# Optimization experiments

Measured on AMD Instinct MI355X. Metric: run time of the kernel, lower is better.

The kernel has to match this reference:

```python
import jax, jax.numpy as jnp
import numpy as np

B, L, S = 1, 2048, 2048
D_MODEL, H = 1024, 16
DK = D_MODEL // H  # d_keys = d_values = 64


def sparsemax(z):
    # sparsemax along last axis: proj of z onto the simplex
    K = z.shape[-1]
    z_sorted = jnp.flip(jnp.sort(z, axis=-1), axis=-1)
    cs = jnp.cumsum(z_sorted, axis=-1)
    r = jnp.arange(1, K + 1, dtype=z.dtype)
    support = 1.0 + r * z_sorted > cs
    k = jnp.sum(support, axis=-1, keepdims=True)
    tau = (jnp.take_along_axis(cs, k.astype(jnp.int32) - 1, axis=-1) - 1.0) / k.astype(z.dtype)
    return jnp.maximum(z - tau, 0.0)


def setup_inputs() -> dict:
    key = jax.random.key(0)
    ks = jax.random.split(key, 12)
    sc = 1.0 / np.sqrt(D_MODEL)
    return {
        "queries": jax.random.normal(ks[0], (B, L, D_MODEL), jnp.float32),
        "keys": jax.random.normal(ks[1], (B, S, D_MODEL), jnp.float32),
        "values": jax.random.normal(ks[2], (B, S, D_MODEL), jnp.float32),
        "Wq": jax.random.normal(ks[3], (D_MODEL, H * DK), jnp.float32) * sc,
        "bq": jnp.zeros((H * DK,), jnp.float32),
        "Wk": jax.random.normal(ks[4], (D_MODEL, H * DK), jnp.float32) * sc,
        "bk": jnp.zeros((H * DK,), jnp.float32),
        "Wv": jax.random.normal(ks[5], (H * DK, H * DK), jnp.float32) * sc,
        "bv": jnp.zeros((H * DK,), jnp.float32),
        "Wo": jax.random.normal(ks[6], (H * DK, D_MODEL), jnp.float32) * sc,
        "bo": jnp.zeros((D_MODEL,), jnp.float32),
    }


def reference(queries, keys, values, Wq, bq, Wk, bk, Wv, bv, Wo, bo):
    # projections (note: input `values` is unused, matching the torch source)
    q = (queries @ Wq + bq).reshape(B, L, H, DK)
    k_flat = keys @ Wk + bk                      # [B,S,H*DK]
    k = k_flat.reshape(B, S, H, DK)
    v = (k_flat @ Wv + bv).reshape(B, S, H, DK)  # value_projection(key_projection(keys))
    scale = 1.0 / np.sqrt(DK)
    scores = jnp.einsum('blhe,bshe->bhls', q, k) * scale  # [B,H,L,S]
    A = sparsemax(scores)
    out = jnp.einsum('bhls,bshd->blhd', A, v)             # [B,L,H,DK]
    # mix=True: transpose(2,1) -> [B,H,L,D] then view(B,L,-1)
    out = jnp.swapaxes(out, 1, 2).reshape(B, L, H * DK)
    return out @ Wo + bo
```

## Files before the change

### kernel.cpp

```cpp
#include <hip/hip_runtime.h>
#include <hip/hip_bf16.h>


typedef __attribute__((ext_vector_type(8))) short short8;
typedef __attribute__((ext_vector_type(4))) float floatx4;

#define SRC_BF16 0
#define SRC_F32  1
#define SRC_RT   2
#define NSEG 3
#define OVF 64
#define CAPT (64 * NSEG + OVF)

typedef __attribute__((address_space(1))) const void GAS;
typedef __attribute__((address_space(3))) void LAS;
#define GLOAD16(g, l) __builtin_amdgcn_global_load_lds((GAS*)(g), (LAS*)(l), 16, 0, 0)

__device__ __forceinline__ short f2bf(float f) {
    __hip_bfloat16 h = __float2bfloat16(f);
    return *reinterpret_cast<const short*>(&h);
}
__device__ __forceinline__ unsigned short f2bfu(float f) {
    __hip_bfloat16 h = __float2bfloat16(f);
    return *reinterpret_cast<const unsigned short*>(&h);
}
__device__ __forceinline__ float bf2f(unsigned short u) {
    return __uint_as_float(((unsigned)u) << 16);
}
__device__ __forceinline__ unsigned fmap(float f) {
    unsigned u = __float_as_uint(f);
    return (u & 0x80000000u) ? ~u : (u | 0x80000000u);
}
__device__ __forceinline__ float funmap(unsigned u) {
    return (u & 0x80000000u) ? __uint_as_float(u ^ 0x80000000u) : __uint_as_float(~u);
}

__global__ void detect_k(const short* __restrict__ q, int n, int* __restrict__ flag)
{
    const int tid = threadIdx.x;
    int bad = 0;
    for (int i = tid; i < n; i += 64) {
        float f = bf2f((unsigned short)q[i]);
        if (!(fabsf(f) < 1e10f)) bad = 1;
    }
    unsigned long long m = __ballot(bad != 0);
    if (tid == 0) *flag = (m != 0ULL) ? 1 : 0;
}

__global__ __launch_bounds__(256)
void convert2_k(const void* __restrict__ s0, const void* __restrict__ s1,
                short* __restrict__ d0, short* __restrict__ d1,
                const int* __restrict__ dflag)
{
    const void* s = blockIdx.z ? s1 : s0;
    short* d = blockIdx.z ? d1 : d0;
    const size_t i = ((size_t)blockIdx.x * 256 + threadIdx.x) * 8;
    short8 o;
    if (*dflag) {
        const float4 f0 = ((const float4*)((const float*)s + i))[0];
        const float4 f1 = ((const float4*)((const float*)s + i))[1];
        o[0] = f2bf(f0.x); o[1] = f2bf(f0.y); o[2] = f2bf(f0.z); o[3] = f2bf(f0.w);
        o[4] = f2bf(f1.x); o[5] = f2bf(f1.y); o[6] = f2bf(f1.z); o[7] = f2bf(f1.w);
    } else {
        o = *(const short8*)((const short*)s + i);
    }
    *(short8*)(d + i) = o;
}

struct TP4 {
    const void* s[4];
    short* d[4];
};
__global__ __launch_bounds__(256)
void transpose4_k(TP4 p, int R, int C, const int* __restrict__ dflag)
{
    __shared__ short T[64][72];
    const int tid = threadIdx.x;
    const int bC = blockIdx.x, bR = blockIdx.y;
    const void* src = p.s[blockIdx.z];
    short* dst = p.d[blockIdx.z];
    const bool f32 = (*dflag != 0);

    const int colg = (tid & 7) * 8;
    #pragma unroll
    for (int h = 0; h < 2; ++h) {
        const int row = (tid >> 3) + 32 * h;
        const size_t idx = (size_t)(bR * 64 + row) * (size_t)C + (size_t)(bC * 64 + colg);
        short e[8];
        if (f32) {
            const float4 f0 = ((const float4*)((const float*)src + idx))[0];
            const float4 f1 = ((const float4*)((const float*)src + idx))[1];
            e[0] = f2bf(f0.x); e[1] = f2bf(f0.y); e[2] = f2bf(f0.z); e[3] = f2bf(f0.w);
            e[4] = f2bf(f1.x); e[5] = f2bf(f1.y); e[6] = f2bf(f1.z); e[7] = f2bf(f1.w);
        } else {
            short8 s = *(const short8*)((const short*)src + idx);
            #pragma unroll
            for (int j = 0; j < 8; ++j) e[j] = s[j];
        }
        #pragma unroll
        for (int j = 0; j < 8; ++j) T[colg + j][row] = e[j];
    }
    __syncthreads();
    #pragma unroll
    for (int h = 0; h < 2; ++h) {
        const int orow = (tid >> 3) + 32 * h;
        const int ocolg = (tid & 7) * 8;
        const size_t idx = (size_t)(bC * 64 + orow) * (size_t)R + (size_t)(bR * 64 + ocolg);
        *(short8*)(dst + idx) = *(const short8*)&T[orow][ocolg];
    }
}

struct GJ { const short* A; const short* B; const void* bias; void* C; float os; };

template<int OSRC>
__global__ __launch_bounds__(256)
void gemm64_bt_k(GJ j0, GJ j1, const int* __restrict__ dflag)
{
    __shared__ __align__(16) short As[2][64][64];
    __shared__ __align__(16) short Bs[2][64][64];

    const GJ j = blockIdx.z ? j1 : j0;
    const int rtf = *dflag;

    const int tid  = threadIdx.x;
    const int bN   = blockIdx.x, bM = blockIdx.y;
    const int lane = tid & 63, wave = tid >> 6;
    const int wm   = (wave >> 1) * 32;
    const int wn   = (wave & 1) * 32;
    const int quad = lane >> 4, r16 = lane & 15;

    floatx4 acc[2][2];
    #pragma unroll
    for (int i = 0; i < 2; ++i)
        #pragma unroll
        for (int jj = 0; jj < 2; ++jj)
            acc[i][jj] = (floatx4){0.f, 0.f, 0.f, 0.f};

    const int srow = wave * 8 + (lane >> 3);
    const int scg  = (lane & 7) ^ ((lane >> 3) & 7);
    const short* gA = j.A + (size_t)(bM * 64 + srow) * 1024 + scg * 8;
    const short* gB = j.B + (size_t)(bN * 64 + srow) * 1024 + scg * 8;

#define STAGE(buf, k0)                                                          \
    {                                                                           \
        _Pragma("unroll")                                                       \
        for (int jj = 0; jj < 2; ++jj) {                                        \
            GLOAD16(gA + (size_t)jj * 32 * 1024 + (k0),                         \
                    &As[buf][wave * 8 + jj * 32][0]);                           \
            GLOAD16(gB + (size_t)jj * 32 * 1024 + (k0),                         \
                    &Bs[buf][wave * 8 + jj * 32][0]);                           \
        }                                                                       \
    }

    STAGE(0, 0);
    __syncthreads();

    const int sr = r16 & 7;
    int buf = 0;
    for (int t = 0; t < 16; ++t) {
        if (t < 15) STAGE(buf ^ 1, (t + 1) * 64);
        #pragma unroll
        for (int kk = 0; kk < 2; ++kk) {
            const int pc = ((kk * 4 + quad) ^ sr) * 8;
            const short8 a0 = *(const short8*)&As[buf][wm + r16][pc];
            const short8 a1 = *(const short8*)&As[buf][wm + 16 + r16][pc];
            const short8 b0 = *(const short8*)&Bs[buf][wn + r16][pc];
            const short8 b1 = *(const short8*)&Bs[buf][wn + 16 + r16][pc];
            acc[0][0] = __builtin_amdgcn_mfma_f32_16x16x32_bf16(a0, b0, acc[0][0], 0, 0, 0);
            acc[0][1] = __builtin_amdgcn_mfma_f32_16x16x32_bf16(a0, b1, acc[0][1], 0, 0, 0);
            acc[1][0] = __builtin_amdgcn_mfma_f32_16x16x32_bf16(a1, b0, acc[1][0], 0, 0, 0);
            acc[1][1] = __builtin_amdgcn_mfma_f32_16x16x32_bf16(a1, b1, acc[1][1], 0, 0, 0);
        }
        __syncthreads();
        buf ^= 1;
    }
#undef STAGE

    const bool of32 = (OSRC == SRC_F32) || (OSRC == SRC_RT && rtf);
    #pragma unroll
    for (int jj = 0; jj < 2; ++jj) {
        const int gc = bN * 64 + wn + jj * 16 + r16;
        const float bb = rtf ? ((const float*)j.bias)[gc]
                             : bf2f(((const unsigned short*)j.bias)[gc]);
        #pragma unroll
        for (int i = 0; i < 2; ++i) {
            #pragma unroll
            for (int rg = 0; rg < 4; ++rg) {
                const int gr = bM * 64 + wm + i * 16 + quad * 4 + rg;
                const float v = (acc[i][jj][rg] + bb) * j.os;
                if (of32)
                    ((float*)j.C)[(size_t)gr * 1024 + gc] = v;
                else
                    ((__hip_bfloat16*)j.C)[(size_t)gr * 1024 + gc] = __float2bfloat16(v);
            }
        }
    }
}

__global__ __launch_bounds__(256, 8)
void attn_fused_k(const short* __restrict__ Qb, const short* __restrict__ Kb,
                  const short* __restrict__ Vb, short* __restrict__ Ob)
{
    __shared__ unsigned cpk[16][CAPT];
    __shared__ unsigned rmax[16];
    __shared__ int cnt[16];

    const int tid  = threadIdx.x;
    const int lane = tid & 63, wave = tid >> 6;
    const int quad = lane >> 4, r16 = lane & 15;

    const int bid  = blockIdx.x;
    const int slot = bid >> 3;
    const int h    = (slot & 1) * 8 + (bid & 7);
    const int row0 = (slot >> 1) * 16;

    if (tid < 16) { rmax[tid] = fmap(-3.0e38f); cnt[tid] = 0; }
    __syncthreads();

    const short* qp = Qb + (size_t)(row0 + r16) * 1024 + h * 64 + quad * 8;
    const short8 qa0 = *(const short8*)qp;
    const short8 qa1 = *(const short8*)(qp + 32);

    const int myrow = quad * 4;
    const int wid   = wave * 16 + r16;
    const short* kp0 = Kb + (size_t)(wave * 16 + r16) * 1024 + h * 64 + quad * 8;

    float rm1[4], rm2[4];
    int mycnt[4];
    #pragma unroll
    for (int rg = 0; rg < 4; ++rg) { rm1[rg] = -3.0e38f; rm2[rg] = -3.0e38f; mycnt[rg] = 0; }

    for (int s0 = 0; s0 < 2048; s0 += 256) {
        floatx4 acc[4];
        #pragma unroll
        for (int t = 0; t < 4; ++t) {
            const short* kp = kp0 + (size_t)(s0 + t * 64) * 1024;
            const short8 b0 = *(const short8*)kp;
            const short8 b1 = *(const short8*)(kp + 32);
            floatx4 a = (floatx4){0.f, 0.f, 0.f, 0.f};
            a = __builtin_amdgcn_mfma_f32_16x16x32_bf16(qa0, b0, a, 0, 0, 0);
            a = __builtin_amdgcn_mfma_f32_16x16x32_bf16(qa1, b1, a, 0, 0, 0);
            acc[t] = a;
        }

        #pragma unroll
        for (int rg = 0; rg < 4; ++rg) {
            float m1ab = fmaxf(acc[0][rg], acc[1][rg]);
            float m2ab = fminf(acc[0][rg], acc[1][rg]);
            float m1cd = fmaxf(acc[2][rg], acc[3][rg]);
            float m2cd = fminf(acc[2][rg], acc[3][rg]);
            float m1 = fmaxf(m1ab, m1cd);
            float m2 = fmaxf(fminf(m1ab, m1cd), (m1ab >= m1cd) ? m2ab : m2cd);
            #pragma unroll
            for (int off = 1; off < 16; off <<= 1) {
                const float o1 = __shfl_xor(m1, off, 64);
                const float o2 = __shfl_xor(m2, off, 64);
                const float n2 = fmaxf(fminf(m1, o1), (m1 >= o1) ? m2 : o2);
                m1 = fmaxf(m1, o1);
                m2 = n2;
            }
            const float n1 = fmaxf(rm1[rg], m1);
            rm2[rg] = fmaxf(fminf(rm1[rg], m1), (rm1[rg] >= m1) ? rm2[rg] : m2);
            rm1[rg] = n1;
            if (r16 == 0) atomicMax(&rmax[myrow + rg], fmap(m1));
        }

        #pragma unroll
        for (int rg = 0; rg < 4; ++rg) {
            const int row = myrow + rg;
            const float g1 = fmaxf(funmap(rmax[row]), rm1[rg]);
            const float thr = fmaxf(g1 - 1.0f, 0.5f * (g1 + rm2[rg]) - 0.5f);
            #pragma unroll
            for (int t = 0; t < 4; ++t) {
                const float val = acc[t][rg];
                if (val >= thr) {
                    const unsigned pk = ((unsigned)f2bfu(val) << 16)
                                      | (unsigned)(s0 + wave * 16 + t * 64 + r16);
                    const int c = mycnt[rg];
                    if (c < NSEG) {
                        cpk[row][wid * NSEG + c] = pk;
                    } else {
                        const int p = atomicAdd(&cnt[row], 1);
                        if (p < OVF) cpk[row][64 * NSEG + p] = pk;
                    }
                    mycnt[rg] = c + 1;
                }
            }
        }
    }

    #pragma unroll
    for (int rg = 0; rg < 4; ++rg) {
        const int row = myrow + rg;
        for (int k = mycnt[rg]; k < NSEG; ++k)
            cpk[row][wid * NSEG + k] = 0xFF800000u;
    }
    __syncthreads();

    const int r = wave * 4 + quad;
    const int novf = min(cnt[r], OVF);

    unsigned ca[16];
    #pragma unroll
    for (int k = 0; k < 12; ++k) ca[k] = cpk[r][k * 16 + r16];
    #pragma unroll
    for (int k = 12; k < 16; ++k) {
        const int oi = k * 16 + r16 - 64 * NSEG;
        ca[k] = (oi < novf) ? cpk[r][k * 16 + r16] : 0xFF800000u;
    }

    float tau = funmap(rmax[r]) - 1.0f;
    float prevc = -1.0f;
    for (int it = 0; it < 18; ++it) {
        float s = 0.f, c = 0.f;
        #pragma unroll
        for (int k = 0; k < 16; ++k) {
            const float v = __uint_as_float(ca[k] & 0xFFFF0000u);
            if (v > tau) { s += v; c += 1.f; }
        }
        #pragma unroll
        for (int off = 1; off < 16; off <<= 1) {
            s += __shfl_xor(s, off, 64);
            c += __shfl_xor(c, off, 64);
        }
        if (c == prevc || c == 0.f) break;
        prevc = c;
        tau = (s - 1.0f) / c;
    }

    const unsigned qpre = (1u << r16) - 1u;
    int base = 0;
    #pragma unroll
    for (int k = 0; k < 16; ++k) {
        const float v = __uint_as_float(ca[k] & 0xFFFF0000u);
        const float p = v - tau;
        const bool keep = (p > 0.f);
        const unsigned long long mm = __ballot(keep);
        const unsigned qm = (unsigned)((mm >> (quad * 16)) & 0xFFFFull);
        if (keep)
            cpk[r][base + __popc(qm & qpre)] =
                ((unsigned)f2bfu(p) << 16) | (ca[k] & 0xFFFFu);
        base += __popc(qm);
    }
    const int msup = base;

    const unsigned short* vb = (const unsigned short*)Vb + (size_t)h * 64 + r16 * 4;
    float o0 = 0.f, o1 = 0.f, o2 = 0.f, o3 = 0.f;
    int jj = 0;
    for (; jj + 2 <= msup; jj += 2) {
        const unsigned ua = cpk[r][jj], ub = cpk[r][jj + 1];
        const float pa = __uint_as_float(ua & 0xFFFF0000u);
        const float pb = __uint_as_float(ub & 0xFFFF0000u);
        const uint2 da = *(const uint2*)(vb + (size_t)(ua & 0xFFFFu) * 1024);
        const uint2 db = *(const uint2*)(vb + (size_t)(ub & 0xFFFFu) * 1024);
        o0 += pa * __uint_as_float(da.x << 16);
        o1 += pa * __uint_as_float(da.x & 0xFFFF0000u);
        o2 += pa * __uint_as_float(da.y << 16);
        o3 += pa * __uint_as_float(da.y & 0xFFFF0000u);
        o0 += pb * __uint_as_float(db.x << 16);
        o1 += pb * __uint_as_float(db.x & 0xFFFF0000u);
        o2 += pb * __uint_as_float(db.y << 16);
        o3 += pb * __uint_as_float(db.y & 0xFFFF0000u);
    }
    if (jj < msup) {
        const unsigned ua = cpk[r][jj];
        const float pa = __uint_as_float(ua & 0xFFFF0000u);
        const uint2 da = *(const uint2*)(vb + (size_t)(ua & 0xFFFFu) * 1024);
        o0 += pa * __uint_as_float(da.x << 16);
        o1 += pa * __uint_as_float(da.x & 0xFFFF0000u);
        o2 += pa * __uint_as_float(da.y << 16);
        o3 += pa * __uint_as_float(da.y & 0xFFFF0000u);
    }

    short* op = Ob + ((size_t)h * 2048 + row0 + r) * 64 + r16 * 4;
    op[0] = f2bf(o0); op[1] = f2bf(o1); op[2] = f2bf(o2); op[3] = f2bf(o3);
}

extern "C" void kernel_launch(void* const* d_in, const int* in_sizes, int n_in,
                              void* d_out, int out_size, void* d_ws, size_t ws_size,
                              hipStream_t stream)
{
    (void)in_sizes; (void)n_in; (void)out_size; (void)ws_size;

    const void* queries = d_in[0];
    const void* keys    = d_in[1];
    const void* Wq = d_in[3];
    const void* bq = d_in[4];
    const void* Wk = d_in[5];
    const void* bk = d_in[6];
    const void* Wv = d_in[7];
    const void* bv = d_in[8];
    const void* Wo = d_in[9];
    const void* bo = d_in[10];

    const int L = 2048, DM = 1024;
    const size_t LD = (size_t)L * DM;

    int*   flag = (int*)d_ws;
    short* Qc  = (short*)((char*)d_ws + 256);
    short* Kc  = Qc + LD;
    short* WqT = Kc + LD;
    short* WkT = WqT + (size_t)DM * DM;
    short* WvT = WkT + (size_t)DM * DM;
    short* WoT = WvT + (size_t)DM * DM;
    short* Qb  = WoT + (size_t)DM * DM;
    short* Kb  = Qb + LD;
    short* Vb  = Kb + LD;
    short* Ob  = Vb + LD;

    dim3 blk(256);

    detect_k<<<dim3(1), dim3(64), 0, stream>>>((const short*)queries, 4096, flag);

    convert2_k<<<dim3((unsigned)(LD / 2048), 1, 2), blk, 0, stream>>>(
        queries, keys, Qc, Kc, flag);

    {
        TP4 p;
        p.s[0] = Wq; p.s[1] = Wk; p.s[2] = Wv; p.s[3] = Wo;
        p.d[0] = WqT; p.d[1] = WkT; p.d[2] = WvT; p.d[3] = WoT;
        transpose4_k<<<dim3(DM / 64, DM / 64, 4), blk, 0, stream>>>(p, DM, DM, flag);
    }

    {
        GJ jq{(const short*)Qc, WqT, bq, Qb, 0.125f};
        GJ jk{(const short*)Kc, WkT, bk, Kb, 1.0f};
        gemm64_bt_k<SRC_BF16><<<dim3(DM / 64, L / 64, 2), blk, 0, stream>>>(jq, jk, flag);
    }
    {
        GJ jv{(const short*)Kb, WvT, bv, Vb, 1.0f};
        gemm64_bt_k<SRC_BF16><<<dim3(DM / 64, L / 64, 1), blk, 0, stream>>>(jv, jv, flag);
    }

    attn_fused_k<<<dim3((L / 16) * 16), blk, 0, stream>>>(Qb, Kb, Vb, Ob);

    {
        GJ jo{(const short*)Ob, WoT, bo, d_out, 1.0f};
        gemm64_bt_k<SRC_RT><<<dim3(DM / 64, L / 64, 1), blk, 0, stream>>>(jo, jo, flag);
    }
}
```

Measured before the change: 264.9 us.

## Transpose score MFMA so each lane owns one query row in candidate selection

Swaps the MFMA operand order so keys form the M dimension and queries the N dimension. Each lane now holds 16 scores for a single query row, so the per-row top-2 tracking becomes a mostly in-register reduction with only two cross-quad shuffles instead of four shuffle rounds per row group. Candidate storage becomes 12 private slots per lane-row with a padded row stride of 257 to reduce LDS bank conflicts. Each wave now scans a contiguous 512-key range, which changes the K access pattern and how the threshold evolves.

```diff
diff --git a/kernel.cpp b/kernel.cpp
--- a/kernel.cpp
+++ b/kernel.cpp
@@ -8,9 +8,10 @@
 #define SRC_BF16 0
 #define SRC_F32  1
 #define SRC_RT   2
-#define NSEG 3
+#define NSEG 12
 #define OVF 64
-#define CAPT (64 * NSEG + OVF)
+#define OVBASE 192
+#define CAPP 257
 
 typedef __attribute__((address_space(1))) const void GAS;
 typedef __attribute__((address_space(3))) void LAS;
@@ -201,7 +202,7 @@
 void attn_fused_k(const short* __restrict__ Qb, const short* __restrict__ Kb,
                   const short* __restrict__ Vb, short* __restrict__ Ob)
 {
-    __shared__ unsigned cpk[16][CAPT];
+    __shared__ unsigned cpk[16][CAPP];
     __shared__ unsigned rmax[16];
     __shared__ int cnt[16];
 
@@ -218,83 +219,77 @@
     __syncthreads();
 
     const short* qp = Qb + (size_t)(row0 + r16) * 1024 + h * 64 + quad * 8;
-    const short8 qa0 = *(const short8*)qp;
-    const short8 qa1 = *(const short8*)(qp + 32);
-
-    const int myrow = quad * 4;
-    const int wid   = wave * 16 + r16;
-    const short* kp0 = Kb + (size_t)(wave * 16 + r16) * 1024 + h * 64 + quad * 8;
-
-    float rm1[4], rm2[4];
-    int mycnt[4];
-    #pragma unroll
-    for (int rg = 0; rg < 4; ++rg) { rm1[rg] = -3.0e38f; rm2[rg] = -3.0e38f; mycnt[rg] = 0; }
-
-    for (int s0 = 0; s0 < 2048; s0 += 256) {
+    const short8 qb0 = *(const short8*)qp;
+    const short8 qb1 = *(const short8*)(qp + 32);
+
+    const int wid   = wave * 4 + quad;
+    const int kbase = wave * 512;
+    const short* kpA = Kb + (size_t)(kbase + r16) * 1024 + h * 64 + quad * 8;
+
+    float rm1 = -3.0e38f, rm2 = -3.0e38f;
+    int mycnt = 0;
+
+    for (int s = 0; s < 8; ++s) {
         floatx4 acc[4];
         #pragma unroll
         for (int t = 0; t < 4; ++t) {
-            const short* kp = kp0 + (size_t)(s0 + t * 64) * 1024;
-            const short8 b0 = *(const short8*)kp;
-            const short8 b1 = *(const short8*)(kp + 32);
+            const short* kp = kpA + (size_t)(s * 64 + t * 16) * 1024;
+            const short8 a0 = *(const short8*)kp;
+            const short8 a1 = *(const short8*)(kp + 32);
             floatx4 a = (floatx4){0.f, 0.f, 0.f, 0.f};
-            a = __builtin_amdgcn_mfma_f32_16x16x32_bf16(qa0, b0, a, 0, 0, 0);
-            a = __builtin_amdgcn_mfma_f32_16x16x32_bf16(qa1, b1, a, 0, 0, 0);
+            a = __builtin_amdgcn_mfma_f32_16x16x32_bf16(a0, qb0, a, 0, 0, 0);
+            a = __builtin_amdgcn_mfma_f32_16x16x32_bf16(a1, qb1, a, 0, 0, 0);
             acc[t] = a;
         }
 
-        #pragma unroll
-        for (int rg = 0; rg < 4; ++rg) {
-            float m1ab = fmaxf(acc[0][rg], acc[1][rg]);
-            float m2ab = fminf(acc[0][rg], acc[1][rg]);
-            float m1cd = fmaxf(acc[2][rg], acc[3][rg]);
-            float m2cd = fminf(acc[2][rg], acc[3][rg]);
-            float m1 = fmaxf(m1ab, m1cd);
-            float m2 = fmaxf(fminf(m1ab, m1cd), (m1ab >= m1cd) ? m2ab : m2cd);
+        float m1 = acc[0][0], m2 = -3.0e38f;
+        #pragma unroll
+        for (int t = 0; t < 4; ++t) {
             #pragma unroll
-            for (int off = 1; off < 16; off <<= 1) {
-                const float o1 = __shfl_xor(m1, off, 64);
-                const float o2 = __shfl_xor(m2, off, 64);
-                const float n2 = fmaxf(fminf(m1, o1), (m1 >= o1) ? m2 : o2);
-                m1 = fmaxf(m1, o1);
-                m2 = n2;
+            for (int rg = 0; rg < 4; ++rg) {
+                if (t == 0 && rg == 0) continue;
+                const float v = acc[t][rg];
+                m2 = fmaxf(m2, fminf(m1, v));
+                m1 = fmaxf(m1, v);
             }
-            const float n1 = fmaxf(rm1[rg], m1);
-            rm2[rg] = fmaxf(fminf(rm1[rg], m1), (rm1[rg] >= m1) ? rm2[rg] : m2);
-            rm1[rg] = n1;
-            if (r16 == 0) atomicMax(&rmax[myrow + rg], fmap(m1));
-        }
-
-        #pragma unroll
-        for (int rg = 0; rg < 4; ++rg) {
-            const int row = myrow + rg;
-            const float g1 = fmaxf(funmap(rmax[row]), rm1[rg]);
-            const float thr = fmaxf(g1 - 1.0f, 0.5f * (g1 + rm2[rg]) - 0.5f);
+        }
+        #pragma unroll
+        for (int off = 16; off < 64; off <<= 1) {
+            const float o1 = __shfl_xor(m1, off, 64);
+            const float o2 = __shfl_xor(m2, off, 64);
+            const float n2 = fmaxf(fminf(m1, o1), (m1 >= o1) ? m2 : o2);
+            m1 = fmaxf(m1, o1);
+            m2 = n2;
+        }
+        rm2 = fmaxf(fminf(rm1, m1), (rm1 >= m1) ? rm2 : m2);
+        rm1 = fmaxf(rm1, m1);
+        if (quad == 0) atomicMax(&rmax[r16], fmap(m1));
+
+        const float g1 = fmaxf(funmap(rmax[r16]), rm1);
+        const float thr = fmaxf(g1 - 1.0f, 0.5f * (g1 + rm2) - 0.5f);
+        #pragma unroll
+        for (int t = 0; t < 4; ++t) {
             #pragma unroll
-            for (int t = 0; t < 4; ++t) {
+            for (int rg = 0; rg < 4; ++rg) {
                 const float val = acc[t][rg];
                 if (val >= thr) {
                     const unsigned pk = ((unsigned)f2bfu(val) << 16)
-                                      | (unsigned)(s0 + wave * 16 + t * 64 + r16);
-                    const int c = mycnt[rg];
+                        | (unsigned)(kbase + s * 64 + t * 16 + quad * 4 + rg);
+                    const int c = mycnt;
                     if (c < NSEG) {
-                        cpk[row][wid * NSEG + c] = pk;
+                        cpk[r16][wid * NSEG + c] = pk;
                     } else {
-                        const int p = atomicAdd(&cnt[row], 1);
-                        if (p < OVF) cpk[row][64 * NSEG + p] = pk;
+                        const int p = atomicAdd(&cnt[r16], 1);
+                        if (p < OVF) cpk[r16][OVBASE + p] = pk;
                     }
-                    mycnt[rg] = c + 1;
+                    mycnt = c + 1;
                 }
             }
         }
     }
 
-    #pragma unroll
-    for (int rg = 0; rg < 4; ++rg) {
-        const int row = myrow + rg;
-        for (int k = mycnt[rg]; k < NSEG; ++k)
-            cpk[row][wid * NSEG + k] = 0xFF800000u;
-    }
+    for (int k = mycnt; k < NSEG; ++k)
+        cpk[r16][wid * NSEG + k] = 0xFF800000u;
     __syncthreads();
 
     const int r = wave * 4 + quad;
@@ -305,7 +300,7 @@
     for (int k = 0; k < 12; ++k) ca[k] = cpk[r][k * 16 + r16];
     #pragma unroll
     for (int k = 12; k < 16; ++k) {
-        const int oi = k * 16 + r16 - 64 * NSEG;
+        const int oi = k * 16 + r16 - OVBASE;
         ca[k] = (oi < novf) ? cpk[r][k * 16 + r16] : 0xFF800000u;
     }
 
```

New measurement: 232.4 us. 1.14x faster.
